# Optimization experiments

Measured on AMD Instinct MI355X. Metric: run time of the kernel, lower is better.

Reference implementation:

```python
import jax, jax.numpy as jnp
import numpy as np

D_MODEL, N_HEADS, D_K, D_V = 1024, 16, 64, 64
B, S = 4, 2048
EPS = 1e-5


def setup_inputs() -> dict:
    key = jax.random.key(0)
    ks = jax.random.split(key, 8)
    scale = 1.0 / np.sqrt(D_MODEL)
    return {
        "input_Q": jax.random.normal(ks[0], (B, S, D_MODEL), dtype=jnp.float32),
        "input_K": jax.random.normal(ks[1], (B, S, D_MODEL), dtype=jnp.float32),
        "input_V": jax.random.normal(ks[2], (B, S, D_MODEL), dtype=jnp.float32),
        "attn_mask": jax.random.bernoulli(ks[3], 0.15, (B, S, S)),  # True = masked
        "W_Q": jax.random.uniform(ks[4], (N_HEADS * D_K, D_MODEL), jnp.float32, -scale, scale),
        "W_K": jax.random.uniform(ks[5], (N_HEADS * D_K, D_MODEL), jnp.float32, -scale, scale),
        "W_V": jax.random.uniform(ks[6], (N_HEADS * D_V, D_MODEL), jnp.float32, -scale, scale),
        "W_fc": jax.random.uniform(ks[7], (D_MODEL, N_HEADS * D_V), jnp.float32, -scale, scale),
    }


def _proj(x, W, h, d):
    # x: [B,S,D] @ W.T ([D, h*d]) -> [B,h,S,d]
    b, s, _ = x.shape
    y = jnp.einsum("bsd,ed->bse", x, W)
    return y.reshape(b, s, h, d).transpose(0, 2, 1, 3)


def reference(input_Q, input_K, input_V, attn_mask, W_Q, W_K, W_V, W_fc):
    b, s, d_model = input_Q.shape
    Q = _proj(input_Q, W_Q, N_HEADS, D_K)  # [B,H,S,dk]
    K = _proj(input_K, W_K, N_HEADS, D_K)
    V = _proj(input_V, W_V, N_HEADS, D_V)

    scores = jnp.einsum("bhqd,bhkd->bhqk", Q, K) / np.sqrt(D_K).astype(np.float32)
    scores = jnp.where(attn_mask[:, None, :, :], jnp.float32(-1e9), scores)
    attn = jax.nn.softmax(scores, axis=-1)  # [B,H,S,S]

    context = jnp.einsum("bhqk,bhkd->bhqd", attn, V)
    context = context.transpose(0, 2, 1, 3).reshape(b, s, N_HEADS * D_V)
    output = jnp.einsum("bse,de->bsd", context, W_fc)

    x = output + input_Q  # residual
    mu = jnp.mean(x, axis=-1, keepdims=True)
    var = jnp.mean(jnp.square(x - mu), axis=-1, keepdims=True)
    ln = (x - mu) / jnp.sqrt(var + EPS)  # fresh LayerNorm: gamma=1, beta=0
    return ln, attn
```

## Files before the change

kernel.cpp:

```cpp
#include <hip/hip_runtime.h>
#include <cstdint>
#include <cstddef>

constexpr int Bc  = 4;
constexpr int Sc  = 2048;
constexpr int DMc = 1024;
constexpr int Hc  = 16;
constexpr int DHc = 64;
constexpr int BHc = Bc * Hc;

typedef float f32x4  __attribute__((ext_vector_type(4)));
typedef short bf16x8 __attribute__((ext_vector_type(8)));

static __device__ __forceinline__ short f2bf(float x) {
  uint32_t u = __builtin_bit_cast(uint32_t, x);
  u += 0x7fffu + ((u >> 16) & 1u);
  return (short)(u >> 16);
}

static __device__ __forceinline__ f32x4 mfma16(bf16x8 a, bf16x8 b, f32x4 c) {
  return __builtin_amdgcn_mfma_f32_16x16x32_bf16(a, b, c, 0, 0, 0);
}

static __device__ __forceinline__ void gload16(const short* g, short* l) {
  __builtin_amdgcn_global_load_lds(
      (const __attribute__((address_space(1))) void*)g,
      (__attribute__((address_space(3))) void*)l, 16, 0, 0);
}

__global__ __launch_bounds__(256) void k_cvt3(const float* __restrict__ a,
                                              const float* __restrict__ b,
                                              const float* __restrict__ c,
                                              short* __restrict__ oa,
                                              short* __restrict__ ob,
                                              short* __restrict__ oc) {
  const float* in = blockIdx.y == 0 ? a : (blockIdx.y == 1 ? b : c);
  short* out      = blockIdx.y == 0 ? oa : (blockIdx.y == 1 ? ob : oc);
  int i = blockIdx.x * 256 + threadIdx.x;
  float4 v = reinterpret_cast<const float4*>(in)[i];
  short4 o;
  o.x = f2bf(v.x); o.y = f2bf(v.y); o.z = f2bf(v.z); o.w = f2bf(v.w);
  reinterpret_cast<short4*>(out)[i] = o;
}

__global__ __launch_bounds__(256) void k_cvtw(const float* __restrict__ a,
                                              const float* __restrict__ b,
                                              const float* __restrict__ c,
                                              const float* __restrict__ d,
                                              short* __restrict__ oa,
                                              short* __restrict__ ob,
                                              short* __restrict__ oc,
                                              short* __restrict__ od) {
  const int y = blockIdx.y;
  const float* in = y == 0 ? a : (y == 1 ? b : (y == 2 ? c : d));
  short* out      = y == 0 ? oa : (y == 1 ? ob : (y == 2 ? oc : od));
  int i = blockIdx.x * 256 + threadIdx.x;
  float4 v = reinterpret_cast<const float4*>(in)[i];
  short4 o;
  o.x = f2bf(v.x); o.y = f2bf(v.y); o.z = f2bf(v.z); o.w = f2bf(v.w);
  reinterpret_cast<short4*>(out)[i] = o;
}

__global__ __launch_bounds__(256) void k_pack(const int* __restrict__ m,
                                              uint32_t* __restrict__ bits) {
  size_t i = (size_t)blockIdx.x * 256 + threadIdx.x;
  uint64_t b = __ballot(m[i] != 0);
  int lane = threadIdx.x & 63;
  if (lane == 0)  bits[i >> 5] = (uint32_t)b;
  if (lane == 32) bits[i >> 5] = (uint32_t)(b >> 32);
}

template <int MODE>
static __device__ __forceinline__ void gemm_body(const short* __restrict__ A,
                                                 const short* __restrict__ Bt,
                                                 void* __restrict__ out,
                                                 int bm, int bn) {
  __shared__ __align__(16) short lA[128 * 64];
  __shared__ __align__(16) short lB[128 * 64];
  const int tid = threadIdx.x;
  const int lane = tid & 63, w = tid >> 6;
  const int wr = w >> 1, wc = w & 1;
  const int r = lane & 15, g = lane >> 4;

  const int lrow8 = lane >> 3;
  const int lsl   = lane & 7;

  f32x4 acc[4][4] = {};
  const short* Ab = A + (size_t)bm * DMc;
  const short* Bb = Bt + (size_t)bn * DMc;

  for (int k0 = 0; k0 < DMc; k0 += 64) {
    __syncthreads();
    #pragma unroll
    for (int rnd = 0; rnd < 4; rnd++) {
      const int row = rnd * 32 + w * 8 + lrow8;
      const int slot = lsl ^ (row & 7);
      gload16(Ab + (size_t)row * DMc + k0 + slot * 8, lA + (rnd * 32 + w * 8) * 64);
      gload16(Bb + (size_t)row * DMc + k0 + slot * 8, lB + (rnd * 32 + w * 8) * 64);
    }
    __syncthreads();

    #pragma unroll
    for (int kk = 0; kk < 2; kk++) {
      bf16x8 af[4], bfr[4];
      #pragma unroll
      for (int i = 0; i < 4; i++) {
        const int arow = wr * 64 + i * 16 + r;
        af[i] = *reinterpret_cast<const bf16x8*>(
            lA + arow * 64 + (((kk * 4 + g) ^ (arow & 7)) << 3));
        const int brow = wc * 64 + i * 16 + r;
        bfr[i] = *reinterpret_cast<const bf16x8*>(
            lB + brow * 64 + (((kk * 4 + g) ^ (brow & 7)) << 3));
      }
      #pragma unroll
      for (int i = 0; i < 4; i++)
        #pragma unroll
        for (int n = 0; n < 4; n++) acc[i][n] = mfma16(af[i], bfr[n], acc[i][n]);
    }
  }

  #pragma unroll
  for (int i = 0; i < 4; i++) {
    #pragma unroll
    for (int n = 0; n < 4; n++) {
      const int col = bn + wc * 64 + n * 16 + r;
      #pragma unroll
      for (int j = 0; j < 4; j++) {
        const int m = bm + wr * 64 + i * 16 + g * 4 + j;
        if (MODE == 2) {
          reinterpret_cast<float*>(out)[(size_t)m * DMc + col] = acc[i][n][j];
        } else {
          const int b = m >> 11, s = m & (Sc - 1);
          const int h = col >> 6, d = col & (DHc - 1);
          size_t idx = (MODE == 1)
              ? ((size_t)(b * Hc + h) * DHc + d) * Sc + s
              : ((size_t)(b * Hc + h) * Sc + s) * DHc + d;
          reinterpret_cast<short*>(out)[idx] = f2bf(acc[i][n][j]);
        }
      }
    }
  }
}

__global__ __launch_bounds__(256) void k_gemmQKV(const short* __restrict__ XQ,
                                                 const short* __restrict__ XK,
                                                 const short* __restrict__ XV,
                                                 const short* __restrict__ WQ,
                                                 const short* __restrict__ WK,
                                                 const short* __restrict__ WV,
                                                 short* __restrict__ Q,
                                                 short* __restrict__ K,
                                                 short* __restrict__ V) {
  const int z = blockIdx.z;
  const int bm = blockIdx.x * 128, bn = blockIdx.y * 128;
  if (z == 0)      gemm_body<0>(XQ, WQ, (void*)Q, bm, bn);
  else if (z == 1) gemm_body<0>(XK, WK, (void*)K, bm, bn);
  else             gemm_body<1>(XV, WV, (void*)V, bm, bn);
}

__global__ __launch_bounds__(256) void k_gemmO(const short* __restrict__ A,
                                               const short* __restrict__ Bt,
                                               float* __restrict__ out) {
  gemm_body<2>(A, Bt, (void*)out, blockIdx.x * 128, blockIdx.y * 128);
}

__global__ __launch_bounds__(512, 4) void k_flash2(const short* __restrict__ Qb,
                                                   const short* __restrict__ Kb,
                                                   const short* __restrict__ Vt,
                                                   const uint32_t* __restrict__ pbits,
                                                   short* __restrict__ ctx,
                                                   float* __restrict__ attn) {
  __shared__ __align__(16) short kbuf[2][4096];
  __shared__ __align__(16) short vbuf[2][4096];
  __shared__ __align__(16) short pbuf[8][1024];

  const int qbase = blockIdx.x * 128;
  const int bh = blockIdx.y;
  const int b = bh >> 4, h = bh & 15;
  const int tid = threadIdx.x;
  const int lane = tid & 63, w = tid >> 6;
  const int r = lane & 15, g = lane >> 4;
  const int rx = r & 7;

  const int srow = tid >> 3;
  const int sslot = (tid & 7) ^ (srow & 7);
  const short* ksrc = Kb + ((size_t)bh * Sc + srow) * DHc + sslot * 8;
  const short* vsrc = Vt + ((size_t)bh * DHc + srow) * Sc + sslot * 8;
  short* const kdst0 = &kbuf[0][w * 512];
  short* const kdst1 = &kbuf[1][w * 512];
  short* const vdst0 = &vbuf[0][w * 512];
  short* const vdst1 = &vbuf[1][w * 512];

  const short* qrow = Qb + ((size_t)bh * Sc + qbase + w * 16 + r) * DHc;
  const bf16x8 qf0 = *reinterpret_cast<const bf16x8*>(qrow + g * 8);
  const bf16x8 qf1 = *reinterpret_cast<const bf16x8*>(qrow + g * 8 + 32);

  const uint32_t* mrow = pbits + ((size_t)b * Sc + qbase + w * 16 + r) * (Sc / 32);

  constexpr float SCL = 0.18033688f;
  f32x4 pacc[4] = {};
  float rs = 0.f;

  gload16(ksrc, kdst0);
  gload16(vsrc, vdst0);
  __syncthreads();

  int cur = 0;
  for (int kt = 0; kt < 32; kt++) {
    if (kt + 1 < 32) {
      gload16(ksrc + (size_t)(kt + 1) * 64 * DHc, cur ? kdst0 : kdst1);
      gload16(vsrc + (kt + 1) * 64,               cur ? vdst0 : vdst1);
    }
    const short* kb = kbuf[cur];
    const short* vb = vbuf[cur];

    f32x4 sc4[4];
    #pragma unroll
    for (int tt = 0; tt < 4; tt++) {
      const int krow = (tt * 16 + r) * 64;
      bf16x8 kf0 = *reinterpret_cast<const bf16x8*>(kb + krow + ((g ^ rx) << 3));
      bf16x8 kf1 = *reinterpret_cast<const bf16x8*>(kb + krow + (((g + 4) ^ rx) << 3));
      f32x4 a = {};
      a = mfma16(kf0, qf0, a);
      a = mfma16(kf1, qf1, a);
      sc4[tt] = a;
    }

    const uint2 mu = *reinterpret_cast<const uint2*>(mrow + kt * 2);
    #pragma unroll
    for (int tt = 0; tt < 4; tt++) {
      const uint32_t mword = (tt < 2) ? mu.x : mu.y;
      const int bsh = (tt & 1) * 16 + g * 4;
      f32x4 e;
      #pragma unroll
      for (int j = 0; j < 4; j++) {
        float v = __builtin_exp2f(sc4[tt][j] * SCL);
        if ((mword >> (bsh + j)) & 1u) v = 0.f;
        e[j] = v;
        rs += v;
      }
      uint32_t lo = (uint32_t)(uint16_t)f2bf(e[0]) | ((uint32_t)(uint16_t)f2bf(e[1]) << 16);
      uint32_t hi = (uint32_t)(uint16_t)f2bf(e[2]) | ((uint32_t)(uint16_t)f2bf(e[3]) << 16);
      uint64_t pk = (uint64_t)lo | ((uint64_t)hi << 32);
      *reinterpret_cast<uint64_t*>(
          &pbuf[w][r * 64 + (((tt * 2 + (g >> 1)) ^ rx) << 3) + ((g & 1) << 2)]) = pk;
    }

    #pragma unroll
    for (int kt2 = 0; kt2 < 2; kt2++) {
      const int sl = ((kt2 * 4 + g) ^ rx) << 3;
      const bf16x8 paf = *reinterpret_cast<const bf16x8*>(&pbuf[w][r * 64 + sl]);
      #pragma unroll
      for (int n = 0; n < 4; n++) {
        const bf16x8 vf = *reinterpret_cast<const bf16x8*>(vb + (n * 16 + r) * 64 + sl);
        pacc[n] = mfma16(paf, vf, pacc[n]);
      }
    }

    __syncthreads();
    cur ^= 1;
  }

  rs += __shfl_xor(rs, 16);
  rs += __shfl_xor(rs, 32);
  const float rinv = 1.0f / rs;

  float riv[4];
  #pragma unroll
  for (int j = 0; j < 4; j++) riv[j] = 1.0f / __shfl(rs, g * 4 + j);

  short* cbase = ctx + ((size_t)b * Sc + qbase + w * 16) * DMc + h * DHc;
  #pragma unroll
  for (int n = 0; n < 4; n++)
    #pragma unroll
    for (int j = 0; j < 4; j++)
      cbase[(size_t)(g * 4 + j) * DMc + n * 16 + r] = f2bf(pacc[n][j] * riv[j]);

  const short* kbase = Kb + (size_t)bh * Sc * DHc;
  float* out = attn + ((size_t)bh * Sc + qbase + w * 16 + r) * Sc;
  #pragma unroll 2
  for (int kt = 0; kt < 32; kt++) {
    const uint2 mu = *reinterpret_cast<const uint2*>(mrow + kt * 2);
    #pragma unroll
    for (int tt = 0; tt < 4; tt++) {
      const short* krow = kbase + (size_t)(kt * 64 + tt * 16 + r) * DHc;
      bf16x8 kf0 = *reinterpret_cast<const bf16x8*>(krow + g * 8);
      bf16x8 kf1 = *reinterpret_cast<const bf16x8*>(krow + g * 8 + 32);
      f32x4 a = {};
      a = mfma16(kf0, qf0, a);
      a = mfma16(kf1, qf1, a);
      const uint32_t mword = (tt < 2) ? mu.x : mu.y;
      const int bsh = (tt & 1) * 16 + g * 4;
      f32x4 o;
      #pragma unroll
      for (int j = 0; j < 4; j++) {
        float v = __builtin_exp2f(a[j] * SCL) * rinv;
        if ((mword >> (bsh + j)) & 1u) v = 0.f;
        o[j] = v;
      }
      __builtin_nontemporal_store(
          o, reinterpret_cast<f32x4*>(out + kt * 64 + tt * 16 + g * 4));
    }
  }
}

__global__ __launch_bounds__(256) void k_ln(const float* __restrict__ y,
                                            const float* __restrict__ resid,
                                            float* __restrict__ out) {
  const int m = blockIdx.x, t = threadIdx.x;
  const float4 a = reinterpret_cast<const float4*>(y + (size_t)m * DMc)[t];
  const float4 b = reinterpret_cast<const float4*>(resid + (size_t)m * DMc)[t];
  float x0 = a.x + b.x, x1 = a.y + b.y, x2 = a.z + b.z, x3 = a.w + b.w;

  float s = x0 + x1 + x2 + x3;
  #pragma unroll
  for (int m2 = 1; m2 < 64; m2 <<= 1) s += __shfl_xor(s, m2);
  __shared__ float red[4];
  __shared__ float red2[4];
  const int w = t >> 6, lane = t & 63;
  if (lane == 0) red[w] = s;
  __syncthreads();
  const float mean = (red[0] + red[1] + red[2] + red[3]) * (1.0f / DMc);

  x0 -= mean; x1 -= mean; x2 -= mean; x3 -= mean;
  float s2 = x0 * x0 + x1 * x1 + x2 * x2 + x3 * x3;
  #pragma unroll
  for (int m2 = 1; m2 < 64; m2 <<= 1) s2 += __shfl_xor(s2, m2);
  if (lane == 0) red2[w] = s2;
  __syncthreads();
  const float var = (red2[0] + red2[1] + red2[2] + red2[3]) * (1.0f / DMc);
  const float rstd = rsqrtf(var + 1e-5f);

  float4 o;
  o.x = x0 * rstd; o.y = x1 * rstd; o.z = x2 * rstd; o.w = x3 * rstd;
  reinterpret_cast<float4*>(out + (size_t)m * DMc)[t] = o;
}

extern "C" void kernel_launch(void* const* d_in, const int* in_sizes, int n_in,
                              void* d_out, int out_size, void* d_ws, size_t ws_size,
                              hipStream_t stream) {
  const float* inQ = (const float*)d_in[0];
  const float* inK = (const float*)d_in[1];
  const float* inV = (const float*)d_in[2];
  const int*   msk = (const int*)d_in[3];
  const float* WQ  = (const float*)d_in[4];
  const float* WK  = (const float*)d_in[5];
  const float* WV  = (const float*)d_in[6];
  const float* Wfc = (const float*)d_in[7];

  float* out_ln   = (float*)d_out;
  float* out_attn = out_ln + (size_t)Bc * Sc * DMc;

  const size_t NX = (size_t)Bc * Sc * DMc;
  const size_t NW = (size_t)DMc * DMc;
  short* ws = (short*)d_ws;
  short* XbQ = ws;
  short* XbK = XbQ + NX;
  short* XbV = XbK + NX;
  short* WQb = XbV + NX;
  short* WKb = WQb + NW;
  short* WVb = WKb + NW;
  short* Wfb = WVb + NW;
  short* Qb  = Wfb + NW;
  short* Kb  = Qb + NX;
  short* Vt  = Kb + NX;
  uint32_t* pbits = (uint32_t*)(Vt + NX);
  short* ctx = XbV;
  float* y   = (float*)XbQ;

  k_cvt3<<<dim3((unsigned)(NX / 1024), 3), 256, 0, stream>>>(inQ, inK, inV, XbQ, XbK, XbV);
  k_cvtw<<<dim3((unsigned)(NW / 1024), 4), 256, 0, stream>>>(WQ, WK, WV, Wfc,
                                                             WQb, WKb, WVb, Wfb);
  k_pack<<<dim3((unsigned)(Bc * Sc * (Sc / 256))), 256, 0, stream>>>(msk, pbits);

  k_gemmQKV<<<dim3(Bc * Sc / 128, DMc / 128, 3), 256, 0, stream>>>(
      XbQ, XbK, XbV, WQb, WKb, WVb, Qb, Kb, Vt);

  k_flash2<<<dim3(Sc / 128, BHc), 512, 0, stream>>>(Qb, Kb, Vt, pbits, ctx, out_attn);

  k_gemmO<<<dim3(Bc * Sc / 128, DMc / 128), 256, 0, stream>>>(ctx, Wfb, y);

  k_ln<<<dim3(Bc * Sc), 256, 0, stream>>>(y, inQ, out_ln);
}
```

Measured before the change: 578.6 us.

## Merge conversion kernels, fuse mask packing into QKV GEMM, restructure attention kernel

Combines the input and weight bf16 conversions into one launch and folds mask bit-packing into the QKV projection launch as extra blocks, reducing launch count and tail idle time. The attention kernel now does a first pass that only computes row sums, then a second pass that recomputes scores, writes normalized probabilities and accumulates P·V using those same normalized values. K and V tiles are read directly from global memory instead of through double-buffered LDS prefetch. Blocks shrink to 256 threads covering 64 queries, which removes block-wide barriers but gives up LDS reuse of K/V and adds uncoalesced global reads for V.

```diff
diff --git a/kernel.cpp b/kernel.cpp
--- a/kernel.cpp
+++ b/kernel.cpp
@@ -28,46 +28,39 @@
       (__attribute__((address_space(3))) void*)l, 16, 0, 0);
 }
 
-__global__ __launch_bounds__(256) void k_cvt3(const float* __restrict__ a,
-                                              const float* __restrict__ b,
-                                              const float* __restrict__ c,
-                                              short* __restrict__ oa,
-                                              short* __restrict__ ob,
-                                              short* __restrict__ oc) {
-  const float* in = blockIdx.y == 0 ? a : (blockIdx.y == 1 ? b : c);
-  short* out      = blockIdx.y == 0 ? oa : (blockIdx.y == 1 ? ob : oc);
-  int i = blockIdx.x * 256 + threadIdx.x;
+__global__ __launch_bounds__(256) void k_cvtall(const float* __restrict__ iQ,
+                                                const float* __restrict__ iK,
+                                                const float* __restrict__ iV,
+                                                const float* __restrict__ wQ,
+                                                const float* __restrict__ wK,
+                                                const float* __restrict__ wV,
+                                                const float* __restrict__ wO,
+                                                short* __restrict__ oQ,
+                                                short* __restrict__ oK,
+                                                short* __restrict__ oV,
+                                                short* __restrict__ owQ,
+                                                short* __restrict__ owK,
+                                                short* __restrict__ owV,
+                                                short* __restrict__ owO) {
+  const int bid = blockIdx.x;
+  const float* in;
+  short* out;
+  int ib;
+  if (bid < 8192)        { in = iQ; out = oQ; ib = bid; }
+  else if (bid < 16384)  { in = iK; out = oK; ib = bid - 8192; }
+  else if (bid < 24576)  { in = iV; out = oV; ib = bid - 16384; }
+  else {
+    const int wb = bid - 24576;
+    const int sel = wb >> 10;
+    in  = sel == 0 ? wQ : (sel == 1 ? wK : (sel == 2 ? wV : wO));
+    out = sel == 0 ? owQ : (sel == 1 ? owK : (sel == 2 ? owV : owO));
+    ib = wb & 1023;
+  }
+  const int i = ib * 256 + threadIdx.x;
   float4 v = reinterpret_cast<const float4*>(in)[i];
   short4 o;
   o.x = f2bf(v.x); o.y = f2bf(v.y); o.z = f2bf(v.z); o.w = f2bf(v.w);
   reinterpret_cast<short4*>(out)[i] = o;
-}
-
-__global__ __launch_bounds__(256) void k_cvtw(const float* __restrict__ a,
-                                              const float* __restrict__ b,
-                                              const float* __restrict__ c,
-                                              const float* __restrict__ d,
-                                              short* __restrict__ oa,
-                                              short* __restrict__ ob,
-                                              short* __restrict__ oc,
-                                              short* __restrict__ od) {
-  const int y = blockIdx.y;
-  const float* in = y == 0 ? a : (y == 1 ? b : (y == 2 ? c : d));
-  short* out      = y == 0 ? oa : (y == 1 ? ob : (y == 2 ? oc : od));
-  int i = blockIdx.x * 256 + threadIdx.x;
-  float4 v = reinterpret_cast<const float4*>(in)[i];
-  short4 o;
-  o.x = f2bf(v.x); o.y = f2bf(v.y); o.z = f2bf(v.z); o.w = f2bf(v.w);
-  reinterpret_cast<short4*>(out)[i] = o;
-}
-
-__global__ __launch_bounds__(256) void k_pack(const int* __restrict__ m,
-                                              uint32_t* __restrict__ bits) {
-  size_t i = (size_t)blockIdx.x * 256 + threadIdx.x;
-  uint64_t b = __ballot(m[i] != 0);
-  int lane = threadIdx.x & 63;
-  if (lane == 0)  bits[i >> 5] = (uint32_t)b;
-  if (lane == 32) bits[i >> 5] = (uint32_t)(b >> 32);
 }
 
 template <int MODE>
@@ -142,143 +135,88 @@
   }
 }
 
-__global__ __launch_bounds__(256) void k_gemmQKV(const short* __restrict__ XQ,
-                                                 const short* __restrict__ XK,
-                                                 const short* __restrict__ XV,
-                                                 const short* __restrict__ WQ,
-                                                 const short* __restrict__ WK,
-                                                 const short* __restrict__ WV,
-                                                 short* __restrict__ Q,
-                                                 short* __restrict__ K,
-                                                 short* __restrict__ V) {
-  const int z = blockIdx.z;
-  const int bm = blockIdx.x * 128, bn = blockIdx.y * 128;
-  if (z == 0)      gemm_body<0>(XQ, WQ, (void*)Q, bm, bn);
-  else if (z == 1) gemm_body<0>(XK, WK, (void*)K, bm, bn);
-  else             gemm_body<1>(XV, WV, (void*)V, bm, bn);
-}
-
-__global__ __launch_bounds__(256) void k_gemmO(const short* __restrict__ A,
-                                               const short* __restrict__ Bt,
-                                               float* __restrict__ out) {
-  gemm_body<2>(A, Bt, (void*)out, blockIdx.x * 128, blockIdx.y * 128);
-}
-
-__global__ __launch_bounds__(512, 4) void k_flash2(const short* __restrict__ Qb,
-                                                   const short* __restrict__ Kb,
-                                                   const short* __restrict__ Vt,
-                                                   const uint32_t* __restrict__ pbits,
-                                                   short* __restrict__ ctx,
-                                                   float* __restrict__ attn) {
-  __shared__ __align__(16) short kbuf[2][4096];
-  __shared__ __align__(16) short vbuf[2][4096];
-  __shared__ __align__(16) short pbuf[8][1024];
-
-  const int qbase = blockIdx.x * 128;
+__global__ __launch_bounds__(256) void k_gemmQKV_pack(
+    const short* __restrict__ XQ, const short* __restrict__ XK,
+    const short* __restrict__ XV, const short* __restrict__ WQ,
+    const short* __restrict__ WK, const short* __restrict__ WV,
+    short* __restrict__ Q, short* __restrict__ K, short* __restrict__ V,
+    const int* __restrict__ msk, uint32_t* __restrict__ bits) {
+  const int bid = blockIdx.x;
+  if (bid < 1536) {
+    const int rem = bid & 511;
+    const int bm = (rem & 63) * 128, bn = (rem >> 6) * 128;
+    const int z = bid >> 9;
+    if (z == 0)      gemm_body<0>(XQ, WQ, (void*)Q, bm, bn);
+    else if (z == 1) gemm_body<0>(XK, WK, (void*)K, bm, bn);
+    else             gemm_body<1>(XV, WV, (void*)V, bm, bn);
+  } else {
+    const size_t wi = (size_t)(bid - 1536) * 256 + threadIdx.x;
+    const uint4* mp = reinterpret_cast<const uint4*>(msk + wi * 32);
+    uint32_t word = 0;
+    #pragma unroll
+    for (int q = 0; q < 8; q++) {
+      const uint4 mv = mp[q];
+      word |= (mv.x != 0 ? 1u : 0u) << (q * 4 + 0);
+      word |= (mv.y != 0 ? 1u : 0u) << (q * 4 + 1);
+      word |= (mv.z != 0 ? 1u : 0u) << (q * 4 + 2);
+      word |= (mv.w != 0 ? 1u : 0u) << (q * 4 + 3);
+    }
+    bits[wi] = word;
+  }
+}
+
+__global__ __launch_bounds__(256) void k_flash2(const short* __restrict__ Qb,
+                                                const short* __restrict__ Kb,
+                                                const short* __restrict__ Vt,
+                                                const uint32_t* __restrict__ pbits,
+                                                short* __restrict__ ctx,
+                                                float* __restrict__ attn) {
+  __shared__ __align__(16) short pbuf[4][1024];
+
   const int bh = blockIdx.y;
   const int b = bh >> 4, h = bh & 15;
-  const int tid = threadIdx.x;
-  const int lane = tid & 63, w = tid >> 6;
+  const int lane = threadIdx.x & 63, w = threadIdx.x >> 6;
   const int r = lane & 15, g = lane >> 4;
   const int rx = r & 7;
-
-  const int srow = tid >> 3;
-  const int sslot = (tid & 7) ^ (srow & 7);
-  const short* ksrc = Kb + ((size_t)bh * Sc + srow) * DHc + sslot * 8;
-  const short* vsrc = Vt + ((size_t)bh * DHc + srow) * Sc + sslot * 8;
-  short* const kdst0 = &kbuf[0][w * 512];
-  short* const kdst1 = &kbuf[1][w * 512];
-  short* const vdst0 = &vbuf[0][w * 512];
-  short* const vdst1 = &vbuf[1][w * 512];
-
-  const short* qrow = Qb + ((size_t)bh * Sc + qbase + w * 16 + r) * DHc;
+  const int q0 = blockIdx.x * 64 + w * 16;
+
+  const short* qrow = Qb + ((size_t)bh * Sc + q0 + r) * DHc;
   const bf16x8 qf0 = *reinterpret_cast<const bf16x8*>(qrow + g * 8);
   const bf16x8 qf1 = *reinterpret_cast<const bf16x8*>(qrow + g * 8 + 32);
 
-  const uint32_t* mrow = pbits + ((size_t)b * Sc + qbase + w * 16 + r) * (Sc / 32);
+  const short* kbase = Kb + (size_t)bh * Sc * DHc;
+  const short* vbase = Vt + (size_t)bh * DHc * Sc;
+  const uint32_t* mrow = pbits + ((size_t)b * Sc + q0 + r) * (Sc / 32);
 
   constexpr float SCL = 0.18033688f;
-  f32x4 pacc[4] = {};
+
   float rs = 0.f;
-
-  gload16(ksrc, kdst0);
-  gload16(vsrc, vdst0);
-  __syncthreads();
-
-  int cur = 0;
   for (int kt = 0; kt < 32; kt++) {
-    if (kt + 1 < 32) {
-      gload16(ksrc + (size_t)(kt + 1) * 64 * DHc, cur ? kdst0 : kdst1);
-      gload16(vsrc + (kt + 1) * 64,               cur ? vdst0 : vdst1);
-    }
-    const short* kb = kbuf[cur];
-    const short* vb = vbuf[cur];
-
-    f32x4 sc4[4];
+    const uint2 mu = *reinterpret_cast<const uint2*>(mrow + kt * 2);
     #pragma unroll
     for (int tt = 0; tt < 4; tt++) {
-      const int krow = (tt * 16 + r) * 64;
-      bf16x8 kf0 = *reinterpret_cast<const bf16x8*>(kb + krow + ((g ^ rx) << 3));
-      bf16x8 kf1 = *reinterpret_cast<const bf16x8*>(kb + krow + (((g + 4) ^ rx) << 3));
+      const short* krow = kbase + (size_t)(kt * 64 + tt * 16 + r) * DHc;
+      bf16x8 kf0 = *reinterpret_cast<const bf16x8*>(krow + g * 8);
+      bf16x8 kf1 = *reinterpret_cast<const bf16x8*>(krow + g * 8 + 32);
       f32x4 a = {};
       a = mfma16(kf0, qf0, a);
       a = mfma16(kf1, qf1, a);
-      sc4[tt] = a;
-    }
-
-    const uint2 mu = *reinterpret_cast<const uint2*>(mrow + kt * 2);
-    #pragma unroll
-    for (int tt = 0; tt < 4; tt++) {
       const uint32_t mword = (tt < 2) ? mu.x : mu.y;
       const int bsh = (tt & 1) * 16 + g * 4;
-      f32x4 e;
       #pragma unroll
       for (int j = 0; j < 4; j++) {
-        float v = __builtin_exp2f(sc4[tt][j] * SCL);
+        float v = __builtin_exp2f(a[j] * SCL);
         if ((mword >> (bsh + j)) & 1u) v = 0.f;
-        e[j] = v;
         rs += v;
       }
-      uint32_t lo = (uint32_t)(uint16_t)f2bf(e[0]) | ((uint32_t)(uint16_t)f2bf(e[1]) << 16);
-      uint32_t hi = (uint32_t)(uint16_t)f2bf(e[2]) | ((uint32_t)(uint16_t)f2bf(e[3]) << 16);
-      uint64_t pk = (uint64_t)lo | ((uint64_t)hi << 32);
-      *reinterpret_cast<uint64_t*>(
-          &pbuf[w][r * 64 + (((tt * 2 + (g >> 1)) ^ rx) << 3) + ((g & 1) << 2)]) = pk;
-    }
-
-    #pragma unroll
-    for (int kt2 = 0; kt2 < 2; kt2++) {
-      const int sl = ((kt2 * 4 + g) ^ rx) << 3;
-      const bf16x8 paf = *reinterpret_cast<const bf16x8*>(&pbuf[w][r * 64 + sl]);
-      #pragma unroll
-      for (int n = 0; n < 4; n++) {
-        const bf16x8 vf = *reinterpret_cast<const bf16x8*>(vb + (n * 16 + r) * 64 + sl);
-        pacc[n] = mfma16(paf, vf, pacc[n]);
-      }
-    }
-
-    __syncthreads();
-    cur ^= 1;
-  }
-
+    }
+  }
   rs += __shfl_xor(rs, 16);
   rs += __shfl_xor(rs, 32);
   const float rinv = 1.0f / rs;
 
-  float riv[4];
-  #pragma unroll
-  for (int j = 0; j < 4; j++) riv[j] = 1.0f / __shfl(rs, g * 4 + j);
-
-  short* cbase = ctx + ((size_t)b * Sc + qbase + w * 16) * DMc + h * DHc;
-  #pragma unroll
-  for (int n = 0; n < 4; n++)
-    #pragma unroll
-    for (int j = 0; j < 4; j++)
-      cbase[(size_t)(g * 4 + j) * DMc + n * 16 + r] = f2bf(pacc[n][j] * riv[j]);
-
-  const short* kbase = Kb + (size_t)bh * Sc * DHc;
-  float* out = attn + ((size_t)bh * Sc + qbase + w * 16 + r) * Sc;
-  #pragma unroll 2
+  f32x4 pacc[4] = {};
+  float* out = attn + ((size_t)bh * Sc + q0 + r) * Sc;
   for (int kt = 0; kt < 32; kt++) {
     const uint2 mu = *reinterpret_cast<const uint2*>(mrow + kt * 2);
     #pragma unroll
@@ -300,8 +238,37 @@
       }
       __builtin_nontemporal_store(
           o, reinterpret_cast<f32x4*>(out + kt * 64 + tt * 16 + g * 4));
-    }
-  }
+      uint32_t lo = (uint32_t)(uint16_t)f2bf(o[0]) | ((uint32_t)(uint16_t)f2bf(o[1]) << 16);
+      uint32_t hi = (uint32_t)(uint16_t)f2bf(o[2]) | ((uint32_t)(uint16_t)f2bf(o[3]) << 16);
+      uint64_t pk = (uint64_t)lo | ((uint64_t)hi << 32);
+      *reinterpret_cast<uint64_t*>(
+          &pbuf[w][r * 64 + (((tt * 2 + (g >> 1)) ^ rx) << 3) + ((g & 1) << 2)]) = pk;
+    }
+    #pragma unroll
+    for (int kk = 0; kk < 2; kk++) {
+      const int sl = ((kk * 4 + g) ^ rx) << 3;
+      const bf16x8 paf = *reinterpret_cast<const bf16x8*>(&pbuf[w][r * 64 + sl]);
+      #pragma unroll
+      for (int n = 0; n < 4; n++) {
+        const bf16x8 vf = *reinterpret_cast<const bf16x8*>(
+            vbase + (size_t)(n * 16 + r) * Sc + kt * 64 + kk * 32 + g * 8);
+        pacc[n] = mfma16(paf, vf, pacc[n]);
+      }
+    }
+  }
+
+  short* cbase = ctx + ((size_t)b * Sc + q0) * DMc + h * DHc;
+  #pragma unroll
+  for (int n = 0; n < 4; n++)
+    #pragma unroll
+    for (int j = 0; j < 4; j++)
+      cbase[(size_t)(g * 4 + j) * DMc + n * 16 + r] = f2bf(pacc[n][j]);
+}
+
+__global__ __launch_bounds__(256) void k_gemmO(const short* __restrict__ A,
+                                               const short* __restrict__ Bt,
+                                               float* __restrict__ out) {
+  gemm_body<2>(A, Bt, (void*)out, blockIdx.x * 128, blockIdx.y * 128);
 }
 
 __global__ __launch_bounds__(256) void k_ln(const float* __restrict__ y,
@@ -368,15 +335,13 @@
   short* ctx = XbV;
   float* y   = (float*)XbQ;
 
-  k_cvt3<<<dim3((unsigned)(NX / 1024), 3), 256, 0, stream>>>(inQ, inK, inV, XbQ, XbK, XbV);
-  k_cvtw<<<dim3((unsigned)(NW / 1024), 4), 256, 0, stream>>>(WQ, WK, WV, Wfc,
-                                                             WQb, WKb, WVb, Wfb);
-  k_pack<<<dim3((unsigned)(Bc * Sc * (Sc / 256))), 256, 0, stream>>>(msk, pbits);
-
-  k_gemmQKV<<<dim3(Bc * Sc / 128, DMc / 128, 3), 256, 0, stream>>>(
-      XbQ, XbK, XbV, WQb, WKb, WVb, Qb, Kb, Vt);
-
-  k_flash2<<<dim3(Sc / 128, BHc), 512, 0, stream>>>(Qb, Kb, Vt, pbits, ctx, out_attn);
+  k_cvtall<<<dim3(28672), 256, 0, stream>>>(inQ, inK, inV, WQ, WK, WV, Wfc,
+                                            XbQ, XbK, XbV, WQb, WKb, WVb, Wfb);
+
+  k_gemmQKV_pack<<<dim3(1536 + 2048), 256, 0, stream>>>(
+      XbQ, XbK, XbV, WQb, WKb, WVb, Qb, Kb, Vt, msk, pbits);
+
+  k_flash2<<<dim3(Sc / 64, BHc), 256, 0, stream>>>(Qb, Kb, Vt, pbits, ctx, out_attn);
 
   k_gemmO<<<dim3(Bc * Sc / 128, DMc / 128), 256, 0, stream>>>(ctx, Wfb, y);
 
```

Result: slower. 909.3 us (+57.2%).
